# Kernel tuning notes

Hardware: AMD Instinct MI355X
Metric: run time of the kernel (lower is better)

## Reference

```python
import jax, jax.numpy as jnp
import numpy as np

B, NQ, NK, D_IN, D_H = 2, 8192, 8192, 256, 256


def setup_inputs() -> dict:
    key = jax.random.key(0)
    ks = jax.random.split(key, 9)
    s = 1.0 / np.sqrt(D_IN)
    return {
        "q": jax.random.normal(ks[0], (B, NQ, D_IN), jnp.float32),
        "k": jax.random.normal(ks[1], (B, NK, D_IN), jnp.float32),
        "v": jax.random.normal(ks[2], (B, NK, D_IN), jnp.float32),
        "Wq": jax.random.uniform(ks[3], (D_IN, D_H), jnp.float32, -s, s),
        "bq": jax.random.uniform(ks[4], (D_H,), jnp.float32, -s, s),
        "Wk": jax.random.uniform(ks[5], (D_IN, D_H), jnp.float32, -s, s),
        "bk": jax.random.uniform(ks[6], (D_H,), jnp.float32, -s, s),
        "Wv": jax.random.uniform(ks[7], (D_IN, D_H), jnp.float32, -s, s),
        "bv": jax.random.uniform(ks[8], (D_H,), jnp.float32, -s, s),
        "chunk_size": 1024,
    }


def reference(q, k, v, Wq, bq, Wk, bk, Wv, bv, chunk_size):
    # Projections (nn.Linear: x @ W + b)
    q_emb = q @ Wq + bq            # [B, NQ, D_H]
    k_emb = k @ Wk + bk            # [B, NK, D_H]
    v_emb = v @ Wv + bv            # value_emb=True -> project v
    # NOTE: original applies NO 1/sqrt(d) scaling.
    # Query chunking in the original is a pure memory optimization;
    # softmax is over the full key axis, so full attention is identical math.
    scores = jnp.einsum("bqd,bkd->bqk", q_emb, k_emb)  # [B, NQ, NK]
    probs = jax.nn.softmax(scores, axis=-1)
    out = jnp.einsum("bqk,bkd->bqd", probs, v_emb)     # [B, NQ, D_H]
    return out
```

## Files before the change

kernel.cpp:

```cpp
#include <hip/hip_runtime.h>

#define B_   2
#define NQ_  8192
#define NK_  8192
#define DIN_ 256
#define DH_  256
#define M_   (B_ * NQ_)

typedef _Float16 f16x8 __attribute__((ext_vector_type(8)));
typedef unsigned short u16x8 __attribute__((ext_vector_type(8)));
typedef unsigned short u16x4 __attribute__((ext_vector_type(4)));
typedef unsigned int  u32x4 __attribute__((ext_vector_type(4)));
typedef float f32x16 __attribute__((ext_vector_type(16)));

__device__ __forceinline__ unsigned short f2h(float f) {
    _Float16 h = (_Float16)f;
    return __builtin_bit_cast(unsigned short, h);
}
__device__ __forceinline__ float h2f(unsigned short u) {
    return (float)__builtin_bit_cast(_Float16, u);
}

__global__ void wt_conv(const float* __restrict__ Wq, const float* __restrict__ Wk,
                        const float* __restrict__ Wv, unsigned short* __restrict__ wt) {
    __shared__ float tile[64][65];
    const int mat = blockIdx.z;
    const int k0 = blockIdx.x * 64, n0 = blockIdx.y * 64;
    const float* W = (mat == 0) ? Wq : (mat == 1) ? Wk : Wv;
#pragma unroll
    for (int p = 0; p < 16; ++p) {
        const int idx = p * 256 + threadIdx.x;
        const int r = idx >> 6, c = idx & 63;
        tile[r][c] = W[(k0 + r) * 256 + n0 + c];
    }
    __syncthreads();
#pragma unroll
    for (int p = 0; p < 16; ++p) {
        const int idx = p * 256 + threadIdx.x;
        const int nr = idx >> 6, kc = idx & 63;
        wt[mat * 65536 + (n0 + nr) * 256 + k0 + kc] = f2h(tile[kc][nr]);
    }
}

__global__ __launch_bounds__(256) void proj(
    const float* __restrict__ xq, const float* __restrict__ xk, const float* __restrict__ xv,
    const float* __restrict__ bq, const float* __restrict__ bk, const float* __restrict__ bv,
    const unsigned short* __restrict__ wt,
    unsigned short* __restrict__ q_emb, unsigned short* __restrict__ k_emb,
    unsigned short* __restrict__ vpack) {
    const int mat = blockIdx.y;
    const float* x    = (mat == 0) ? xq : (mat == 1) ? xk : xv;
    const float* bias = (mat == 0) ? bq : (mat == 1) ? bk : bv;
    const unsigned short* w = wt + mat * 65536;

    const int tid = threadIdx.x;
    const int l = tid & 63, wv = tid >> 6;
    const int pair = wv >> 1, h = wv & 1;
    const int lm = l & 31, lh = l >> 5;
    const int row0 = blockIdx.x * 64;
    const int m = row0 + pair * 32 + lm;

    f32x16 acc[4];
#pragma unroll
    for (int i = 0; i < 4; ++i)
#pragma unroll
        for (int j = 0; j < 16; ++j) acc[i][j] = 0.0f;

#pragma unroll
    for (int ks = 0; ks < 16; ++ks) {
        const float4* ap = (const float4*)(x + (size_t)m * 256 + ks * 16 + lh * 8);
        float4 a0 = ap[0], a1 = ap[1];
        u16x8 au;
        au[0] = f2h(a0.x); au[1] = f2h(a0.y); au[2] = f2h(a0.z); au[3] = f2h(a0.w);
        au[4] = f2h(a1.x); au[5] = f2h(a1.y); au[6] = f2h(a1.z); au[7] = f2h(a1.w);
        f16x8 af = __builtin_bit_cast(f16x8, au);
#pragma unroll
        for (int nt = 0; nt < 4; ++nt) {
            f16x8 bfr = *(const f16x8*)(w + (h * 128 + nt * 32 + lm) * 256 + ks * 16 + lh * 8);
            acc[nt] = __builtin_amdgcn_mfma_f32_32x32x16_f16(af, bfr, acc[nt], 0, 0, 0);
        }
    }

    if (mat < 2) {
        unsigned short* emb = (mat == 0) ? q_emb : k_emb;
#pragma unroll
        for (int nt = 0; nt < 4; ++nt) {
            const int n = h * 128 + nt * 32 + lm;
            const float bsv = bias[n];
#pragma unroll
            for (int r = 0; r < 16; ++r) {
                const int rl = (r & 3) + 8 * (r >> 2) + 4 * lh;
                emb[(size_t)(row0 + pair * 32 + rl) * 256 + n] = f2h(acc[nt][r] + bsv);
            }
        }
    } else {
        const int batch = row0 >> 13;
        const int m0 = (row0 & 8191) + pair * 32;
        unsigned short* vp = vpack + (size_t)batch * (512 * 8 * 64 * 8);
        const int base_kt = m0 >> 4;
#pragma unroll
        for (int nt = 0; nt < 4; ++nt) {
            const int dg = h * 4 + nt;
            const int n = h * 128 + nt * 32 + lm;
            const float bsv = bias[n];
#pragma unroll
            for (int g = 0; g < 4; ++g) {
                u16x4 pk;
#pragma unroll
                for (int i = 0; i < 4; ++i) pk[i] = f2h(acc[nt][4 * g + i] + bsv);
                const int kt = base_kt + (g >> 1);
                const int lane = (g & 1) * 32 + lm;
                *(u16x4*)(vp + ((size_t)(kt * 8 + dg) * 64 + lane) * 8 + lh * 4) = pk;
            }
        }
    }
}

#define BN_ 128
#define NT_ (NK_ / BN_)
#define KB_BYTES 65536
#define PSTRIDE 272
#define PBYTES  (64 * PSTRIDE)
#define STAT_OFF (2 * KB_BYTES + PBYTES)
#define LDS_TOTAL (STAT_OFF + 2048)

__global__ __launch_bounds__(512, 2) void flash(
    const unsigned short* __restrict__ q_emb, const unsigned short* __restrict__ k_emb,
    const unsigned short* __restrict__ vpack, float* __restrict__ out) {
    __shared__ __align__(16) char lds_raw[LDS_TOTAL];
    char* pbuf = lds_raw + 2 * KB_BYTES;
    float* smax = (float*)(lds_raw + STAT_OFF);
    float* ssum = smax + 256;
    float* alph = ssum + 256;
    float* linvb = alph + 64;

    const int tid = threadIdx.x;
    const int l = tid & 63, wv = tid >> 6;
    const int kq = wv >> 1, pair = wv & 1;
    const int lm = l & 31, lh = l >> 5;

    const int bx = blockIdx.x;
    const int batch = bx >> 7;
    const int qb = (bx & 127) * 64;

    const unsigned short* kg = k_emb + (size_t)batch * NK_ * 256;
    const unsigned short* vp = vpack + (size_t)batch * (512 * 8 * 64 * 8);

    const int mrow = batch * NQ_ + qb + pair * 32 + lm;
    f16x8 qf[16];
#pragma unroll
    for (int ks = 0; ks < 16; ++ks)
        qf[ks] = *(const f16x8*)(q_emb + (size_t)mrow * 256 + ks * 16 + lh * 8);

    f32x16 oacc[2];
#pragma unroll
    for (int i = 0; i < 2; ++i)
#pragma unroll
        for (int j = 0; j < 16; ++j) oacc[i][j] = 0.0f;

    float mstat = -3.0e38f, lstat = 0.0f;

    const int rlane = l >> 5;
    const int gl = l & 31;
    auto stage_k = [&](int kb, char* kdst) {
#pragma unroll
        for (int p = 0; p < 8; ++p) {
            const int r0 = wv * 16 + 2 * p;
            const int r = r0 + rlane;
            const int gsw = gl ^ (r & 31);
            const unsigned short* src = kg + (size_t)(kb + r) * 256 + gsw * 8;
            __builtin_amdgcn_global_load_lds(
                (const __attribute__((address_space(1))) void*)src,
                (__attribute__((address_space(3))) void*)(kdst + r0 * 512),
                16, 0, 0);
        }
    };

    f16x8 vf[8];
    auto load_v = [&](int kb) {
        const size_t kt0 = (size_t)(kb >> 4);
#pragma unroll
        for (int ks2 = 0; ks2 < 8; ++ks2)
            vf[ks2] = *(const f16x8*)(vp + (((kt0 + ks2) * 8 + wv) * 64 + l) * 8);
    };

    stage_k(0, lds_raw);
    __syncthreads();

    const int prow = pair * 32 + lm;

    for (int t = 0; t < NT_; ++t) {
        const int kb = t * BN_;
        char* kcur = lds_raw + (t & 1) * KB_BYTES;
        if (t + 1 < NT_) stage_k(kb + BN_, lds_raw + ((t + 1) & 1) * KB_BYTES);
        load_v(kb);

        f32x16 s;
#pragma unroll
        for (int j = 0; j < 16; ++j) s[j] = 0.0f;
#pragma unroll
        for (int ks = 0; ks < 16; ++ks) {
            const int gsw = (2 * ks + lh) ^ lm;
            f16x8 kf = *(const f16x8*)(kcur + (kq * 32 + lm) * 512 + gsw * 16);
            s = __builtin_amdgcn_mfma_f32_32x32x16_f16(kf, qf[ks], s, 0, 0, 0);
        }

        float pm = s[0];
#pragma unroll
        for (int j = 1; j < 16; ++j) pm = fmaxf(pm, s[j]);
        pm = fmaxf(pm, __shfl_xor(pm, 32, 64));
        if (lh == 0) smax[prow * 4 + kq] = pm;
        __syncthreads();

        const float4 m4 = *(const float4*)&smax[prow * 4];
        const float gm = fmaxf(fmaxf(m4.x, m4.y), fmaxf(m4.z, m4.w));
        const float mn = fmaxf(mstat, gm);
        const float alpha = __expf(mstat - mn);
        mstat = mn;
        if (kq == 0 && lh == 0) alph[prow] = alpha;

        float psum = 0.0f;
#pragma unroll
        for (int g = 0; g < 4; ++g) {
            u16x4 pk;
#pragma unroll
            for (int j = 0; j < 4; ++j) {
                const unsigned short hh = f2h(__expf(s[g * 4 + j] - mn));
                pk[j] = hh;
                psum += h2f(hh);
            }
            *(u16x4*)(pbuf + prow * PSTRIDE + (kq * 32 + 8 * g + 4 * lh) * 2) = pk;
        }
        psum += __shfl_xor(psum, 32, 64);
        if (lh == 0) ssum[prow * 4 + kq] = psum;
        __syncthreads();

        const float4 s4 = *(const float4*)&ssum[prow * 4];
        lstat = lstat * alpha + (s4.x + s4.y) + (s4.z + s4.w);

        const float a0 = alph[lm];
        const float a1 = alph[lm + 32];
#pragma unroll
        for (int j = 0; j < 16; ++j) oacc[0][j] *= a0;
#pragma unroll
        for (int j = 0; j < 16; ++j) oacc[1][j] *= a1;

#pragma unroll
        for (int ks2 = 0; ks2 < 8; ++ks2) {
            const f16x8 vfr = vf[ks2];
            f16x8 pf0 = *(const f16x8*)(pbuf + lm * PSTRIDE + ks2 * 32 + lh * 16);
            f16x8 pf1 = *(const f16x8*)(pbuf + (lm + 32) * PSTRIDE + ks2 * 32 + lh * 16);
            oacc[0] = __builtin_amdgcn_mfma_f32_32x32x16_f16(vfr, pf0, oacc[0], 0, 0, 0);
            oacc[1] = __builtin_amdgcn_mfma_f32_32x32x16_f16(vfr, pf1, oacc[1], 0, 0, 0);
        }
    }

    if (kq == 0 && lh == 0) linvb[prow] = 1.0f / lstat;
    __syncthreads();
    const float linv0 = linvb[lm];
    const float linv1 = linvb[lm + 32];
#pragma unroll
    for (int qt = 0; qt < 2; ++qt) {
        const float lv = qt ? linv1 : linv0;
        float* orow = out + (size_t)(batch * NQ_ + qb + qt * 32 + lm) * 256 + wv * 32;
#pragma unroll
        for (int g = 0; g < 4; ++g) {
            float4 o4;
            o4.x = oacc[qt][4 * g + 0] * lv;
            o4.y = oacc[qt][4 * g + 1] * lv;
            o4.z = oacc[qt][4 * g + 2] * lv;
            o4.w = oacc[qt][4 * g + 3] * lv;
            *(float4*)(orow + 8 * g + 4 * lh) = o4;
        }
    }
}

extern "C" void kernel_launch(void* const* d_in, const int* in_sizes, int n_in,
                              void* d_out, int out_size, void* d_ws, size_t ws_size,
                              hipStream_t stream) {
    const float* q  = (const float*)d_in[0];
    const float* k  = (const float*)d_in[1];
    const float* v  = (const float*)d_in[2];
    const float* Wq = (const float*)d_in[3];
    const float* bq = (const float*)d_in[4];
    const float* Wk = (const float*)d_in[5];
    const float* bk = (const float*)d_in[6];
    const float* Wv = (const float*)d_in[7];
    const float* bv = (const float*)d_in[8];
    float* out = (float*)d_out;

    unsigned short* wt      = (unsigned short*)d_ws;
    unsigned short* q_emb   = wt + 3 * 65536;
    unsigned short* k_emb   = q_emb + (size_t)M_ * DH_;
    unsigned short* vpack   = k_emb + (size_t)M_ * DH_;

    wt_conv<<<dim3(4, 4, 3), 256, 0, stream>>>(Wq, Wk, Wv, wt);
    proj<<<dim3(256, 3), 256, 0, stream>>>(q, k, v, bq, bk, bv, wt, q_emb, k_emb, vpack);
    flash<<<256, 512, 0, stream>>>(q_emb, k_emb, vpack, out);
}
```

Before: 314.7 us.

## Pre-pack weights in MFMA fragment order and stage X tile through LDS

The weight conversion kernel now writes fp16 weights in the exact per-lane MFMA fragment order, so proj loads each B fragment as one contiguous 16-byte-per-lane access. The proj kernel first loads its 64x256 input tile with coalesced float4 reads, converts to fp16 once into XOR-swizzled shared memory, then reads A fragments from LDS. This avoids each wave pair reloading and reconverting the same strided input rows, but adds 32KB of LDS per block and a barrier. Only the projection stage changes; the flash kernel is untouched.

```diff
diff --git a/kernel.cpp b/kernel.cpp
--- a/kernel.cpp
+++ b/kernel.cpp
@@ -22,7 +22,7 @@
 }
 
 __global__ void wt_conv(const float* __restrict__ Wq, const float* __restrict__ Wk,
-                        const float* __restrict__ Wv, unsigned short* __restrict__ wt) {
+                        const float* __restrict__ Wv, unsigned short* __restrict__ wpack) {
     __shared__ float tile[64][65];
     const int mat = blockIdx.z;
     const int k0 = blockIdx.x * 64, n0 = blockIdx.y * 64;
@@ -34,31 +34,57 @@
         tile[r][c] = W[(k0 + r) * 256 + n0 + c];
     }
     __syncthreads();
-#pragma unroll
-    for (int p = 0; p < 16; ++p) {
-        const int idx = p * 256 + threadIdx.x;
-        const int nr = idx >> 6, kc = idx & 63;
-        wt[mat * 65536 + (n0 + nr) * 256 + k0 + kc] = f2h(tile[kc][nr]);
+    unsigned short* wp = wpack + mat * 65536;
+#pragma unroll
+    for (int p = 0; p < 2; ++p) {
+        const int e = p * 256 + threadIdx.x;
+        const int kk8 = e >> 6;
+        const int nn = e & 63;
+        const int ks = (k0 >> 4) + (kk8 >> 1);
+        const int lh = kk8 & 1;
+        const int ng = (n0 >> 5) + (nn >> 5);
+        const int l = (nn & 31) + 32 * lh;
+        u16x8 val;
+#pragma unroll
+        for (int j = 0; j < 8; ++j) val[j] = f2h(tile[kk8 * 8 + j][nn]);
+        *(u16x8*)(wp + ((size_t)(ks * 8 + ng) * 64 + l) * 8) = val;
     }
 }
 
 __global__ __launch_bounds__(256) void proj(
     const float* __restrict__ xq, const float* __restrict__ xk, const float* __restrict__ xv,
     const float* __restrict__ bq, const float* __restrict__ bk, const float* __restrict__ bv,
-    const unsigned short* __restrict__ wt,
+    const unsigned short* __restrict__ wpack,
     unsigned short* __restrict__ q_emb, unsigned short* __restrict__ k_emb,
     unsigned short* __restrict__ vpack) {
+    __shared__ __align__(16) unsigned short xt[64 * 256];
     const int mat = blockIdx.y;
     const float* x    = (mat == 0) ? xq : (mat == 1) ? xk : xv;
     const float* bias = (mat == 0) ? bq : (mat == 1) ? bk : bv;
-    const unsigned short* w = wt + mat * 65536;
+    const unsigned short* wp = wpack + mat * 65536;
 
     const int tid = threadIdx.x;
     const int l = tid & 63, wv = tid >> 6;
     const int pair = wv >> 1, h = wv & 1;
     const int lm = l & 31, lh = l >> 5;
     const int row0 = blockIdx.x * 64;
-    const int m = row0 + pair * 32 + lm;
+
+    {
+        const float* xb = x + (size_t)row0 * 256;
+#pragma unroll
+        for (int p = 0; p < 8; ++p) {
+            const int idx = p * 256 + tid;
+            const int r = idx >> 5;
+            const int c8 = idx & 31;
+            const float4* ap = (const float4*)(xb + r * 256 + c8 * 8);
+            float4 a0 = ap[0], a1 = ap[1];
+            u16x8 au;
+            au[0] = f2h(a0.x); au[1] = f2h(a0.y); au[2] = f2h(a0.z); au[3] = f2h(a0.w);
+            au[4] = f2h(a1.x); au[5] = f2h(a1.y); au[6] = f2h(a1.z); au[7] = f2h(a1.w);
+            *(u16x8*)(xt + r * 256 + (c8 ^ (r & 31)) * 8) = au;
+        }
+    }
+    __syncthreads();
 
     f32x16 acc[4];
 #pragma unroll
@@ -68,15 +94,11 @@
 
 #pragma unroll
     for (int ks = 0; ks < 16; ++ks) {
-        const float4* ap = (const float4*)(x + (size_t)m * 256 + ks * 16 + lh * 8);
-        float4 a0 = ap[0], a1 = ap[1];
-        u16x8 au;
-        au[0] = f2h(a0.x); au[1] = f2h(a0.y); au[2] = f2h(a0.z); au[3] = f2h(a0.w);
-        au[4] = f2h(a1.x); au[5] = f2h(a1.y); au[6] = f2h(a1.z); au[7] = f2h(a1.w);
-        f16x8 af = __builtin_bit_cast(f16x8, au);
+        f16x8 af = *(const f16x8*)(xt + (pair * 32 + lm) * 256 +
+                                   (((ks * 2 + lh) ^ lm) * 8));
 #pragma unroll
         for (int nt = 0; nt < 4; ++nt) {
-            f16x8 bfr = *(const f16x8*)(w + (h * 128 + nt * 32 + lm) * 256 + ks * 16 + lh * 8);
+            f16x8 bfr = *(const f16x8*)(wp + ((size_t)(ks * 8 + h * 4 + nt) * 64 + l) * 8);
             acc[nt] = __builtin_amdgcn_mfma_f32_32x32x16_f16(af, bfr, acc[nt], 0, 0, 0);
         }
     }
@@ -289,12 +311,12 @@
     const float* bv = (const float*)d_in[8];
     float* out = (float*)d_out;
 
-    unsigned short* wt      = (unsigned short*)d_ws;
-    unsigned short* q_emb   = wt + 3 * 65536;
+    unsigned short* wpack   = (unsigned short*)d_ws;
+    unsigned short* q_emb   = wpack + 3 * 65536;
     unsigned short* k_emb   = q_emb + (size_t)M_ * DH_;
     unsigned short* vpack   = k_emb + (size_t)M_ * DH_;
 
-    wt_conv<<<dim3(4, 4, 3), 256, 0, stream>>>(Wq, Wk, Wv, wt);
-    proj<<<dim3(256, 3), 256, 0, stream>>>(q, k, v, bq, bk, bv, wt, q_emb, k_emb, vpack);
+    wt_conv<<<dim3(4, 4, 3), 256, 0, stream>>>(Wq, Wk, Wv, wpack);
+    proj<<<dim3(256, 3), 256, 0, stream>>>(q, k, v, bq, bk, bv, wpack, q_emb, k_emb, vpack);
     flash<<<256, 512, 0, stream>>>(q_emb, k_emb, vpack, out);
 }
```

New measurement: 286.3 us. 9.0% less time.
